# Kernel tuning notes

Hardware: AMD Instinct MI355X
Metric: run time of the kernel (lower is better)

Reference implementation:

```python
import jax, jax.numpy as jnp
import numpy as np

EPS = 1e-8  # torch nn.CosineSimilarity default eps


def setup_inputs() -> dict:
    key = jax.random.key(0)
    k1, k2, k3 = jax.random.split(key, 3)
    N, K, Q, CH, H, W, D = 32, 5, 15, 3, 84, 84, 1600
    supp_x = jax.random.normal(k1, (N, K, CH, H, W), dtype=jnp.float32)
    query_x = jax.random.normal(k2, (N, Q, CH, H, W), dtype=jnp.float32)
    W_enc = jax.random.normal(k3, (CH * H * W, D), dtype=jnp.float32) * 0.02
    return {"supp_x": supp_x, "query_x": query_x, "W_enc": W_enc}


def reference(supp_x, query_x, W_enc):
    N, K = supp_x.shape[0], supp_x.shape[1]
    Q = query_x.shape[1]
    # encoder: flatten image -> linear projection (stands in for backbone)
    s_feat = supp_x.reshape(N * K, -1) @ W_enc          # (N*K, D)
    x_proto = s_feat.reshape(N, K, -1).mean(axis=1)     # (N, D) class prototypes
    x_q = query_x.reshape(N * Q, -1) @ W_enc            # (N*Q, D)
    # cosine similarity: L2-normalize with eps clamp, then single matmul
    qn = x_q / jnp.maximum(jnp.linalg.norm(x_q, axis=1, keepdims=True), EPS)
    pn = x_proto / jnp.maximum(jnp.linalg.norm(x_proto, axis=1, keepdims=True), EPS)
    sim = qn @ pn.T                                     # (N*Q, N)
    return jax.nn.log_softmax(sim, axis=1)
```

## Files before the change

### kernel.cpp

```cpp
#include <hip/hip_runtime.h>
#include <hip/hip_bf16.h>
#include <cstdint>
#include <cstddef>

namespace {

constexpr int NCLS   = 32;
constexpr int KSHOT  = 5;
constexpr int FDIM   = 21168;
constexpr int KPAD   = 21248;
constexpr int DDIM   = 1600;
constexpr int NROW   = 512;
constexpr int NQROW  = 480;
constexpr int NKT    = 332;
constexpr int MAXS   = 18;

using short8 = __attribute__((ext_vector_type(8))) short;
using f32x4  = __attribute__((ext_vector_type(4))) float;

__device__ __forceinline__ unsigned short f2bf(float x) {
    union { float f; unsigned u; } v; v.f = x;
    unsigned r = v.u + 0x7fffu + ((v.u >> 16) & 1u);
    return (unsigned short)(r >> 16);
}

__device__ __forceinline__ unsigned short f2bfc(float x) {
    __hip_bfloat16 h = __float2bfloat16(x);
    unsigned short u;
    __builtin_memcpy(&u, &h, 2);
    return u;
}

__device__ __forceinline__ float bf2f(unsigned short u) {
    union { unsigned u; float f; } v; v.u = (unsigned)u << 16;
    return v.f;
}

__global__ void prep_A(const float* __restrict__ supp,
                       const float* __restrict__ query,
                       unsigned short* __restrict__ A) {
    const int r = blockIdx.y;
    const int u = blockIdx.x * blockDim.x + threadIdx.x;
    if (u >= KPAD / 4) return;
    const int c = u * 4;
    float4 v = make_float4(0.f, 0.f, 0.f, 0.f);
    if (c < FDIM) {
        if (r < NCLS) {
            const float* s = supp + (size_t)r * KSHOT * FDIM + c;
            float4 a0 = *(const float4*)(s);
            float4 a1 = *(const float4*)(s + FDIM);
            float4 a2 = *(const float4*)(s + 2 * FDIM);
            float4 a3 = *(const float4*)(s + 3 * FDIM);
            float4 a4 = *(const float4*)(s + 4 * FDIM);
            v.x = (a0.x + a1.x + a2.x + a3.x + a4.x) * 0.2f;
            v.y = (a0.y + a1.y + a2.y + a3.y + a4.y) * 0.2f;
            v.z = (a0.z + a1.z + a2.z + a3.z + a4.z) * 0.2f;
            v.w = (a0.w + a1.w + a2.w + a3.w + a4.w) * 0.2f;
        } else {
            v = *(const float4*)(query + (size_t)(r - NCLS) * FDIM + c);
        }
    }
    ushort4 o;
    o.x = f2bf(v.x); o.y = f2bf(v.y); o.z = f2bf(v.z); o.w = f2bf(v.w);
    *(ushort4*)(A + (size_t)r * KPAD + c) = o;
}

__global__ __launch_bounds__(1024, 4) void gemm15(
        const unsigned short* __restrict__ A,
        const float* __restrict__ W,
        unsigned short* __restrict__ Cpart, int S) {
    __shared__ unsigned short Al[2][256 * 64];
    __shared__ unsigned short Bl[2][256 * 64];

    const int nwg = gridDim.x, orig = blockIdx.x;
    const int xcd = orig & 7, q8 = nwg >> 3, r8 = nwg & 7;
    const int wgid = (xcd < r8 ? xcd * (q8 + 1) : r8 * (q8 + 1) + (xcd - r8) * q8)
                   + (orig >> 3);

    const int s   = wgid / 14;
    const int rem = wgid % 14;
    const int mt  = rem & 1;
    const int nt  = rem >> 1;
    const int m0  = mt * 256;
    const int n0  = nt * 256;
    const int t0  = (NKT * s) / S;
    const int t1  = (NKT * (s + 1)) / S;
    const int tmax = t1 - 1;

    const int tid  = threadIdx.x;
    const int lane = tid & 63;
    const int w    = tid >> 6;
    const int wr   = w & 3;
    const int wc   = w >> 2;
    const int g    = lane >> 4;
    const int r15  = lane & 15;

    const int srow = lane >> 3, sblk = lane & 7;
    const unsigned short* Asrc[2];
    int AdstOff[2];
    #pragma unroll
    for (int i = 0; i < 2; ++i) {
        const int r = w * 16 + i * 8 + srow;
        Asrc[i] = A + (size_t)(m0 + r) * KPAD + (size_t)((sblk ^ (r & 7)) * 8);
        AdstOff[i] = (w * 16 + i * 8) * 64;
    }

    const int bcol = tid & 255;
    const int kseg = tid >> 8;
    const int ncb  = min(n0 + bcol, DDIM - 1);
    const float* Wp = W + ncb;
    const int wb0 = bcol * 64 + (((2 * kseg + 0) ^ (bcol & 7)) * 8);
    const int wb1 = bcol * 64 + (((2 * kseg + 1) ^ (bcol & 7)) * 8);

    f32x4 acc[4][4];
    #pragma unroll
    for (int i = 0; i < 4; ++i)
        #pragma unroll
        for (int j = 0; j < 4; ++j)
            acc[i][j] = (f32x4){0.f, 0.f, 0.f, 0.f};

    float wv[16];

#define LOAD_W(t) { const int kb_ = (t) * 64 + kseg * 16; _Pragma("unroll") \
    for (int i = 0; i < 16; ++i) { \
        const int k_ = kb_ + i; \
        wv[i] = (k_ < FDIM) ? Wp[(size_t)k_ * DDIM] : 0.f; } }

#define PACK_B(buf) { uint4 P0, P1; \
    P0.x = f2bfc(wv[0])  | ((unsigned)f2bfc(wv[1])  << 16); \
    P0.y = f2bfc(wv[2])  | ((unsigned)f2bfc(wv[3])  << 16); \
    P0.z = f2bfc(wv[4])  | ((unsigned)f2bfc(wv[5])  << 16); \
    P0.w = f2bfc(wv[6])  | ((unsigned)f2bfc(wv[7])  << 16); \
    P1.x = f2bfc(wv[8])  | ((unsigned)f2bfc(wv[9])  << 16); \
    P1.y = f2bfc(wv[10]) | ((unsigned)f2bfc(wv[11]) << 16); \
    P1.z = f2bfc(wv[12]) | ((unsigned)f2bfc(wv[13]) << 16); \
    P1.w = f2bfc(wv[14]) | ((unsigned)f2bfc(wv[15]) << 16); \
    *(uint4*)&Bl[buf][wb0] = P0; \
    *(uint4*)&Bl[buf][wb1] = P1; }

#define GLDS_A(buf, t) { _Pragma("unroll") \
    for (int i = 0; i < 2; ++i) \
        __builtin_amdgcn_global_load_lds( \
            (const __attribute__((address_space(1))) void*)(Asrc[i] + (size_t)(t) * 64), \
            (__attribute__((address_space(3))) void*)(&Al[buf][AdstOff[i]]), 16, 0, 0); }

#define COMPUTE(buf) { _Pragma("unroll") \
    for (int kk = 0; kk < 2; ++kk) { \
        const int q_ = kk * 4 + g; \
        short8 bf_[4]; \
        _Pragma("unroll") \
        for (int ns = 0; ns < 4; ++ns) { \
            const int n_ = wc * 64 + ns * 16 + r15; \
            bf_[ns] = *(const short8*)&Bl[buf][n_ * 64 + ((q_ ^ (n_ & 7)) * 8)]; \
        } \
        _Pragma("unroll") \
        for (int ms = 0; ms < 4; ++ms) { \
            const int R_ = wr * 64 + ms * 16 + r15; \
            short8 af_ = *(const short8*)&Al[buf][R_ * 64 + ((q_ ^ (R_ & 7)) * 8)]; \
            _Pragma("unroll") \
            for (int ns = 0; ns < 4; ++ns) \
                acc[ms][ns] = __builtin_amdgcn_mfma_f32_16x16x32_bf16( \
                    af_, bf_[ns], acc[ms][ns], 0, 0, 0); } } }

    LOAD_W(t0);
    PACK_B(0);
    LOAD_W(min(t0 + 1, tmax));
    GLDS_A(0, t0);
    __syncthreads();

    int cur = 0;
    for (int t = t0; t < t1; ++t) {
        const bool m1 = (t + 1 < t1);
        if (m1) {
            PACK_B(cur ^ 1);
            LOAD_W(min(t + 2, tmax));
            GLDS_A(cur ^ 1, t + 1);
        }
        COMPUTE(cur);
        __syncthreads();
        if (m1) cur ^= 1;
    }

#undef LOAD_W
#undef PACK_B
#undef GLDS_A
#undef COMPUTE

    unsigned short* Cp = Cpart + (size_t)s * NROW * DDIM;
    #pragma unroll
    for (int ms = 0; ms < 4; ++ms) {
        const int row = m0 + wr * 64 + ms * 16 + g * 4;
        #pragma unroll
        for (int ns = 0; ns < 4; ++ns) {
            const int col = n0 + wc * 64 + ns * 16 + r15;
            if (col < DDIM) {
                #pragma unroll
                for (int r = 0; r < 4; ++r)
                    Cp[(size_t)(row + r) * DDIM + col] = f2bfc(acc[ms][ns][r]);
            }
        }
    }
}

__global__ void reduce_norm(const unsigned short* __restrict__ Cpart,
                            float* __restrict__ C,
                            float* __restrict__ inv_norm, int S) {
    const int row = blockIdx.x;
    const int tid = threadIdx.x;
    float acc = 0.f;
    for (int c4 = tid * 4; c4 < DDIM; c4 += 1024) {
        float4 v = make_float4(0.f, 0.f, 0.f, 0.f);
        for (int s2 = 0; s2 < S; ++s2) {
            ushort4 u = *(const ushort4*)&Cpart[((size_t)s2 * NROW + row) * DDIM + c4];
            v.x += bf2f(u.x); v.y += bf2f(u.y);
            v.z += bf2f(u.z); v.w += bf2f(u.w);
        }
        *(float4*)&C[(size_t)row * DDIM + c4] = v;
        acc += v.x * v.x + v.y * v.y + v.z * v.z + v.w * v.w;
    }
    __shared__ float red[4];
    #pragma unroll
    for (int off = 32; off > 0; off >>= 1) acc += __shfl_xor(acc, off);
    if ((tid & 63) == 0) red[tid >> 6] = acc;
    __syncthreads();
    if (tid == 0) {
        float a = red[0] + red[1] + red[2] + red[3];
        inv_norm[row] = 1.f / fmaxf(sqrtf(a), 1e-8f);
    }
}

__global__ void simlog(const float* __restrict__ C,
                       const float* __restrict__ inv_norm,
                       float* __restrict__ out) {
    __shared__ float qs[DDIM];
    __shared__ float sims[NCLS];
    const int r = blockIdx.x;
    const int tid = threadIdx.x;
    const float* qrow = C + (size_t)(NCLS + r) * DDIM;
    for (int c = tid; c < DDIM; c += 256) qs[c] = qrow[c];
    __syncthreads();
    const float invq = inv_norm[NCLS + r];
    const int lane = tid & 63, w = tid >> 6;
    #pragma unroll
    for (int j = 0; j < 8; ++j) {
        const int p = w * 8 + j;
        const float* prow = C + (size_t)p * DDIM;
        float d = 0.f;
        for (int c = lane; c < DDIM; c += 64) d += qs[c] * prow[c];
        #pragma unroll
        for (int off = 32; off > 0; off >>= 1) d += __shfl_xor(d, off);
        if (lane == 0) sims[p] = d * invq * inv_norm[p];
    }
    __syncthreads();
    if (w == 0) {
        float v = (lane < NCLS) ? sims[lane] : -1e30f;
        float m = v;
        #pragma unroll
        for (int off = 32; off > 0; off >>= 1) m = fmaxf(m, __shfl_xor(m, off));
        float e = (lane < NCLS) ? expf(v - m) : 0.f;
        float ss = e;
        #pragma unroll
        for (int off = 32; off > 0; off >>= 1) ss += __shfl_xor(ss, off);
        if (lane < NCLS) out[(size_t)r * NCLS + lane] = v - m - logf(ss);
    }
}

}


extern "C" void kernel_launch(void* const* d_in, const int* in_sizes, int n_in,
                              void* d_out, int out_size, void* d_ws, size_t ws_size,
                              hipStream_t stream) {
    const float* supp  = (const float*)d_in[0];
    const float* query = (const float*)d_in[1];
    const float* Wenc  = (const float*)d_in[2];
    float* out = (float*)d_out;

    const size_t fixedA = 21757952;
    const size_t slotBf = (size_t)NROW * DDIM * 2;
    const size_t slotC  = (size_t)NROW * DDIM * 4;

    int S = MAXS;
    if (ws_size > fixedA + slotC + 4096) {
        size_t avail = (ws_size - fixedA - slotC - 4096) / slotBf;
        if ((size_t)S > avail) S = (int)avail;
    }
    if (S < 1) S = 1;

    char* ws = (char*)d_ws;
    unsigned short* A = (unsigned short*)ws;
    unsigned short* Cpart = (unsigned short*)(ws + fixedA);
    float* C        = (float*)(ws + fixedA + (size_t)S * slotBf);
    float* inv_norm = (float*)(ws + fixedA + (size_t)S * slotBf + slotC);

    hipLaunchKernelGGL(prep_A, dim3((KPAD / 4 + 255) / 256, NROW), dim3(256),
                       0, stream, supp, query, A);
    hipLaunchKernelGGL(gemm15, dim3(14 * S), dim3(1024), 0, stream,
                       A, Wenc, Cpart, S);
    hipLaunchKernelGGL(reduce_norm, dim3(NROW), dim3(256), 0, stream,
                       Cpart, C, inv_norm, S);
    hipLaunchKernelGGL(simlog, dim3(NQROW), dim3(256), 0, stream,
                       C, inv_norm, out);
}
```

Before: 141.2 us.

## Split GEMM main loop into four barrier-synced MFMA phases with interleaved loads

The K-tile loop of the encoder GEMM is restructured into four phases per tile, each loading a small set of A/B fragments, hitting a workgroup barrier, and issuing its MFMAs at raised wave priority via s_setprio. The next tile's W loads are split into two halves, and the bf16 pack is placed between phases so global latency and LDS writes overlap with matrix work. An explicit vmcnt/lgkmcnt wait is used instead of __syncthreads. W prefetch distance drops from two tiles to one, which can expose more global-load latency, and the extra barriers add synchronisation cost.

```diff
diff --git a/kernel.cpp b/kernel.cpp
--- a/kernel.cpp
+++ b/kernel.cpp
@@ -65,12 +65,12 @@
     *(ushort4*)(A + (size_t)r * KPAD + c) = o;
 }
 
-__global__ __launch_bounds__(1024, 4) void gemm15(
+__global__ __launch_bounds__(1024, 4) void gemm17(
         const unsigned short* __restrict__ A,
         const float* __restrict__ W,
         unsigned short* __restrict__ Cpart, int S) {
-    __shared__ unsigned short Al[2][256 * 64];
-    __shared__ unsigned short Bl[2][256 * 64];
+    __shared__ unsigned short Abuf[2][256 * 64];
+    __shared__ unsigned short Bbuf[2][256 * 64];
 
     const int nwg = gridDim.x, orig = blockIdx.x;
     const int xcd = orig & 7, q8 = nwg >> 3, r8 = nwg & 7;
@@ -92,7 +92,7 @@
     const int w    = tid >> 6;
     const int wr   = w & 3;
     const int wc   = w >> 2;
-    const int g    = lane >> 4;
+    const int gl   = lane >> 4;
     const int r15  = lane & 15;
 
     const int srow = lane >> 3, sblk = lane & 7;
@@ -121,8 +121,13 @@
 
     float wv[16];
 
-#define LOAD_W(t) { const int kb_ = (t) * 64 + kseg * 16; _Pragma("unroll") \
-    for (int i = 0; i < 16; ++i) { \
+#define LOAD_W_LO(t) { const int kb_ = (t) * 64 + kseg * 16; _Pragma("unroll") \
+    for (int i = 0; i < 8; ++i) { \
+        const int k_ = kb_ + i; \
+        wv[i] = (k_ < FDIM) ? Wp[(size_t)k_ * DDIM] : 0.f; } }
+
+#define LOAD_W_HI(t) { const int kb_ = (t) * 64 + kseg * 16; _Pragma("unroll") \
+    for (int i = 8; i < 16; ++i) { \
         const int k_ = kb_ + i; \
         wv[i] = (k_ < FDIM) ? Wp[(size_t)k_ * DDIM] : 0.f; } }
 
@@ -135,61 +140,74 @@
     P1.y = f2bfc(wv[10]) | ((unsigned)f2bfc(wv[11]) << 16); \
     P1.z = f2bfc(wv[12]) | ((unsigned)f2bfc(wv[13]) << 16); \
     P1.w = f2bfc(wv[14]) | ((unsigned)f2bfc(wv[15]) << 16); \
-    *(uint4*)&Bl[buf][wb0] = P0; \
-    *(uint4*)&Bl[buf][wb1] = P1; }
+    *(uint4*)&Bbuf[buf][wb0] = P0; \
+    *(uint4*)&Bbuf[buf][wb1] = P1; }
 
 #define GLDS_A(buf, t) { _Pragma("unroll") \
     for (int i = 0; i < 2; ++i) \
         __builtin_amdgcn_global_load_lds( \
             (const __attribute__((address_space(1))) void*)(Asrc[i] + (size_t)(t) * 64), \
-            (__attribute__((address_space(3))) void*)(&Al[buf][AdstOff[i]]), 16, 0, 0); }
-
-#define COMPUTE(buf) { _Pragma("unroll") \
-    for (int kk = 0; kk < 2; ++kk) { \
-        const int q_ = kk * 4 + g; \
-        short8 bf_[4]; \
+            (__attribute__((address_space(3))) void*)(&Abuf[buf][AdstOff[i]]), 16, 0, 0); }
+
+#define PHASE(buf, KK, MH, ENDWAIT) { \
+    const int q_ = (KK) * 4 + gl; \
+    short8 af_[2], bf_[4]; \
+    _Pragma("unroll") \
+    for (int mi = 0; mi < 2; ++mi) { \
+        const int R_ = wr * 64 + (2 * (MH) + mi) * 16 + r15; \
+        af_[mi] = *(const short8*)&Abuf[buf][R_ * 64 + ((q_ ^ (R_ & 7)) * 8)]; \
+    } \
+    _Pragma("unroll") \
+    for (int ns = 0; ns < 4; ++ns) { \
+        const int n_ = wc * 64 + ns * 16 + r15; \
+        bf_[ns] = *(const short8*)&Bbuf[buf][n_ * 64 + ((q_ ^ (n_ & 7)) * 8)]; \
+    } \
+    ENDWAIT; \
+    __builtin_amdgcn_s_barrier(); \
+    __builtin_amdgcn_s_setprio(1); \
+    _Pragma("unroll") \
+    for (int mi = 0; mi < 2; ++mi) \
         _Pragma("unroll") \
-        for (int ns = 0; ns < 4; ++ns) { \
-            const int n_ = wc * 64 + ns * 16 + r15; \
-            bf_[ns] = *(const short8*)&Bl[buf][n_ * 64 + ((q_ ^ (n_ & 7)) * 8)]; \
-        } \
-        _Pragma("unroll") \
-        for (int ms = 0; ms < 4; ++ms) { \
-            const int R_ = wr * 64 + ms * 16 + r15; \
-            short8 af_ = *(const short8*)&Al[buf][R_ * 64 + ((q_ ^ (R_ & 7)) * 8)]; \
-            _Pragma("unroll") \
-            for (int ns = 0; ns < 4; ++ns) \
-                acc[ms][ns] = __builtin_amdgcn_mfma_f32_16x16x32_bf16( \
-                    af_, bf_[ns], acc[ms][ns], 0, 0, 0); } } }
-
-    LOAD_W(t0);
+        for (int ns = 0; ns < 4; ++ns) \
+            acc[2 * (MH) + mi][ns] = __builtin_amdgcn_mfma_f32_16x16x32_bf16( \
+                af_[mi], bf_[ns], acc[2 * (MH) + mi][ns], 0, 0, 0); \
+    __builtin_amdgcn_s_setprio(0); }
+
+#define NOWAIT
+#define TILEWAIT asm volatile("s_waitcnt vmcnt(0) lgkmcnt(0)" ::: "memory")
+
+    LOAD_W_LO(t0); LOAD_W_HI(t0);
     PACK_B(0);
-    LOAD_W(min(t0 + 1, tmax));
     GLDS_A(0, t0);
-    __syncthreads();
+    TILEWAIT;
+    __builtin_amdgcn_s_barrier();
 
     int cur = 0;
     for (int t = t0; t < t1; ++t) {
-        const bool m1 = (t + 1 < t1);
-        if (m1) {
-            PACK_B(cur ^ 1);
-            LOAD_W(min(t + 2, tmax));
-            GLDS_A(cur ^ 1, t + 1);
-        }
-        COMPUTE(cur);
-        __syncthreads();
-        if (m1) cur ^= 1;
-    }
-
-#undef LOAD_W
+        const int tn = min(t + 1, tmax);
+        GLDS_A(cur ^ 1, tn);
+        LOAD_W_LO(tn);
+        PHASE(cur, 0, 0, NOWAIT);
+        LOAD_W_HI(tn);
+        PHASE(cur, 0, 1, NOWAIT);
+        PACK_B(cur ^ 1);
+        PHASE(cur, 1, 0, NOWAIT);
+        PHASE(cur, 1, 1, TILEWAIT);
+        cur ^= 1;
+    }
+
+#undef LOAD_W_LO
+#undef LOAD_W_HI
 #undef PACK_B
 #undef GLDS_A
-#undef COMPUTE
+#undef PHASE
+#undef NOWAIT
+#undef TILEWAIT
 
     unsigned short* Cp = Cpart + (size_t)s * NROW * DDIM;
     #pragma unroll
     for (int ms = 0; ms < 4; ++ms) {
-        const int row = m0 + wr * 64 + ms * 16 + g * 4;
+        const int row = m0 + wr * 64 + ms * 16 + gl * 4;
         #pragma unroll
         for (int ns = 0; ns < 4; ++ns) {
             const int col = n0 + wc * 64 + ns * 16 + r15;
@@ -295,7 +313,7 @@
 
     hipLaunchKernelGGL(prep_A, dim3((KPAD / 4 + 255) / 256, NROW), dim3(256),
                        0, stream, supp, query, A);
-    hipLaunchKernelGGL(gemm15, dim3(14 * S), dim3(1024), 0, stream,
+    hipLaunchKernelGGL(gemm17, dim3(14 * S), dim3(1024), 0, stream,
                        A, Wenc, Cpart, S);
     hipLaunchKernelGGL(reduce_norm, dim3(NROW), dim3(256), 0, stream,
                        Cpart, C, inv_norm, S);
```

After: 216.0 us. 53.0% more time.

## Vectorize W loads as float2 and reorder GEMM pipeline with ping-pong register buffers

Applied to the files above, without the earlier changes.

W is now loaded two columns at a time as float2, with each thread covering 8 k-values for 2 columns instead of 16 k-values for one column. This halves the number of global load instructions and changes the LDS swizzle to match. The main loop is unrolled by two and uses two register buffers. The next A tile load and W load are issued before the MFMA compute, and B packing moves to after the compute, so load latency overlaps with math. In exchange, register pressure goes up, and the new swizzle may change LDS bank conflicts.

```diff
diff --git a/kernel.cpp b/kernel.cpp
--- a/kernel.cpp
+++ b/kernel.cpp
@@ -65,12 +65,12 @@
     *(ushort4*)(A + (size_t)r * KPAD + c) = o;
 }
 
-__global__ __launch_bounds__(1024, 4) void gemm15(
+__global__ __launch_bounds__(1024, 4) void gemm18(
         const unsigned short* __restrict__ A,
         const float* __restrict__ W,
         unsigned short* __restrict__ Cpart, int S) {
-    __shared__ unsigned short Al[2][256 * 64];
-    __shared__ unsigned short Bl[2][256 * 64];
+    __shared__ unsigned short Abuf[2][256 * 64];
+    __shared__ unsigned short Bbuf[2][256 * 64];
 
     const int nwg = gridDim.x, orig = blockIdx.x;
     const int xcd = orig & 7, q8 = nwg >> 3, r8 = nwg & 7;
@@ -92,7 +92,7 @@
     const int w    = tid >> 6;
     const int wr   = w & 3;
     const int wc   = w >> 2;
-    const int g    = lane >> 4;
+    const int gl   = lane >> 4;
     const int r15  = lane & 15;
 
     const int srow = lane >> 3, sblk = lane & 7;
@@ -105,12 +105,12 @@
         AdstOff[i] = (w * 16 + i * 8) * 64;
     }
 
-    const int bcol = tid & 255;
-    const int kseg = tid >> 8;
-    const int ncb  = min(n0 + bcol, DDIM - 1);
+    const int c2   = (tid & 127) * 2;
+    const int kseg = tid >> 7;
+    const int ncb  = min(n0 + c2, DDIM - 2);
     const float* Wp = W + ncb;
-    const int wb0 = bcol * 64 + (((2 * kseg + 0) ^ (bcol & 7)) * 8);
-    const int wb1 = bcol * 64 + (((2 * kseg + 1) ^ (bcol & 7)) * 8);
+    const int wg0 = (c2 + 0) * 64 + ((kseg ^ ((c2 >> 1) & 7)) * 8);
+    const int wg1 = wg0 + 64;
 
     f32x4 acc[4][4];
     #pragma unroll
@@ -119,66 +119,74 @@
         for (int j = 0; j < 4; ++j)
             acc[i][j] = (f32x4){0.f, 0.f, 0.f, 0.f};
 
-    float wv[16];
-
-#define LOAD_W(t) { const int kb_ = (t) * 64 + kseg * 16; _Pragma("unroll") \
-    for (int i = 0; i < 16; ++i) { \
+    float2 wvA[8], wvB[8];
+
+#define LOAD_W(wv, t) { const int kb_ = (t) * 64 + kseg * 8; _Pragma("unroll") \
+    for (int i = 0; i < 8; ++i) { \
         const int k_ = kb_ + i; \
-        wv[i] = (k_ < FDIM) ? Wp[(size_t)k_ * DDIM] : 0.f; } }
-
-#define PACK_B(buf) { uint4 P0, P1; \
-    P0.x = f2bfc(wv[0])  | ((unsigned)f2bfc(wv[1])  << 16); \
-    P0.y = f2bfc(wv[2])  | ((unsigned)f2bfc(wv[3])  << 16); \
-    P0.z = f2bfc(wv[4])  | ((unsigned)f2bfc(wv[5])  << 16); \
-    P0.w = f2bfc(wv[6])  | ((unsigned)f2bfc(wv[7])  << 16); \
-    P1.x = f2bfc(wv[8])  | ((unsigned)f2bfc(wv[9])  << 16); \
-    P1.y = f2bfc(wv[10]) | ((unsigned)f2bfc(wv[11]) << 16); \
-    P1.z = f2bfc(wv[12]) | ((unsigned)f2bfc(wv[13]) << 16); \
-    P1.w = f2bfc(wv[14]) | ((unsigned)f2bfc(wv[15]) << 16); \
-    *(uint4*)&Bl[buf][wb0] = P0; \
-    *(uint4*)&Bl[buf][wb1] = P1; }
+        wv[i] = (k_ < FDIM) ? *(const float2*)(Wp + (size_t)k_ * DDIM) \
+                            : make_float2(0.f, 0.f); } }
+
+#define PACK_B(buf, wv) { uint4 P0, P1; \
+    P0.x = f2bfc(wv[0].x) | ((unsigned)f2bfc(wv[1].x) << 16); \
+    P0.y = f2bfc(wv[2].x) | ((unsigned)f2bfc(wv[3].x) << 16); \
+    P0.z = f2bfc(wv[4].x) | ((unsigned)f2bfc(wv[5].x) << 16); \
+    P0.w = f2bfc(wv[6].x) | ((unsigned)f2bfc(wv[7].x) << 16); \
+    P1.x = f2bfc(wv[0].y) | ((unsigned)f2bfc(wv[1].y) << 16); \
+    P1.y = f2bfc(wv[2].y) | ((unsigned)f2bfc(wv[3].y) << 16); \
+    P1.z = f2bfc(wv[4].y) | ((unsigned)f2bfc(wv[5].y) << 16); \
+    P1.w = f2bfc(wv[6].y) | ((unsigned)f2bfc(wv[7].y) << 16); \
+    *(uint4*)&Bbuf[buf][wg0] = P0; \
+    *(uint4*)&Bbuf[buf][wg1] = P1; }
 
 #define GLDS_A(buf, t) { _Pragma("unroll") \
     for (int i = 0; i < 2; ++i) \
         __builtin_amdgcn_global_load_lds( \
             (const __attribute__((address_space(1))) void*)(Asrc[i] + (size_t)(t) * 64), \
-            (__attribute__((address_space(3))) void*)(&Al[buf][AdstOff[i]]), 16, 0, 0); }
+            (__attribute__((address_space(3))) void*)(&Abuf[buf][AdstOff[i]]), 16, 0, 0); }
 
 #define COMPUTE(buf) { _Pragma("unroll") \
     for (int kk = 0; kk < 2; ++kk) { \
-        const int q_ = kk * 4 + g; \
+        const int q_ = kk * 4 + gl; \
         short8 bf_[4]; \
         _Pragma("unroll") \
         for (int ns = 0; ns < 4; ++ns) { \
             const int n_ = wc * 64 + ns * 16 + r15; \
-            bf_[ns] = *(const short8*)&Bl[buf][n_ * 64 + ((q_ ^ (n_ & 7)) * 8)]; \
+            bf_[ns] = *(const short8*)&Bbuf[buf][n_ * 64 + ((q_ ^ ((n_ >> 1) & 7)) * 8)]; \
         } \
         _Pragma("unroll") \
         for (int ms = 0; ms < 4; ++ms) { \
             const int R_ = wr * 64 + ms * 16 + r15; \
-            short8 af_ = *(const short8*)&Al[buf][R_ * 64 + ((q_ ^ (R_ & 7)) * 8)]; \
+            short8 af_ = *(const short8*)&Abuf[buf][R_ * 64 + ((q_ ^ (R_ & 7)) * 8)]; \
             _Pragma("unroll") \
             for (int ns = 0; ns < 4; ++ns) \
                 acc[ms][ns] = __builtin_amdgcn_mfma_f32_16x16x32_bf16( \
                     af_, bf_[ns], acc[ms][ns], 0, 0, 0); } } }
 
-    LOAD_W(t0);
-    PACK_B(0);
-    LOAD_W(min(t0 + 1, tmax));
+    LOAD_W(wvA, t0);
+    PACK_B(0, wvA);
     GLDS_A(0, t0);
+    LOAD_W(wvA, min(t0 + 1, tmax));
     __syncthreads();
 
     int cur = 0;
-    for (int t = t0; t < t1; ++t) {
-        const bool m1 = (t + 1 < t1);
-        if (m1) {
-            PACK_B(cur ^ 1);
-            LOAD_W(min(t + 2, tmax));
-            GLDS_A(cur ^ 1, t + 1);
-        }
+    int t = t0;
+    for (; t + 1 < t1; t += 2) {
+        GLDS_A(cur ^ 1, t + 1);
+        LOAD_W(wvB, min(t + 2, tmax));
         COMPUTE(cur);
+        PACK_B(cur ^ 1, wvA);
         __syncthreads();
-        if (m1) cur ^= 1;
+        cur ^= 1;
+        GLDS_A(cur ^ 1, min(t + 2, tmax));
+        LOAD_W(wvA, min(t + 3, tmax));
+        COMPUTE(cur);
+        PACK_B(cur ^ 1, wvB);
+        __syncthreads();
+        cur ^= 1;
+    }
+    if (t < t1) {
+        COMPUTE(cur);
     }
 
 #undef LOAD_W
@@ -189,7 +197,7 @@
     unsigned short* Cp = Cpart + (size_t)s * NROW * DDIM;
     #pragma unroll
     for (int ms = 0; ms < 4; ++ms) {
-        const int row = m0 + wr * 64 + ms * 16 + g * 4;
+        const int row = m0 + wr * 64 + ms * 16 + gl * 4;
         #pragma unroll
         for (int ns = 0; ns < 4; ++ns) {
             const int col = n0 + wc * 64 + ns * 16 + r15;
@@ -295,7 +303,7 @@
 
     hipLaunchKernelGGL(prep_A, dim3((KPAD / 4 + 255) / 256, NROW), dim3(256),
                        0, stream, supp, query, A);
-    hipLaunchKernelGGL(gemm15, dim3(14 * S), dim3(1024), 0, stream,
+    hipLaunchKernelGGL(gemm18, dim3(14 * S), dim3(1024), 0, stream,
                        A, Wenc, Cpart, S);
     hipLaunchKernelGGL(reduce_norm, dim3(NROW), dim3(256), 0, stream,
                        Cpart, C, inv_norm, S);
```

Result: slower. 306.3 us (+116.9%).
